# Optimization experiments

Measured on AMD Instinct MI355X. Metric: run time of the kernel, lower is better.

The kernel has to match this reference:

```python
import jax, jax.numpy as jnp
import numpy as np

L, D, H, DFF, P, B = 10, 512, 8, 1536, 16, 1024
DK = D // H
SQRT_DK = float(np.sqrt(DK))

# board geometry constants (square index -> rank/file/diag)
_pos = np.arange(64)
FILES = _pos % 8
RANKS = _pos // 8
DIAGS = RANKS + FILES
ADIAGS = RANKS - FILES + 7
RIDX = np.clip(RANKS[:, None] - RANKS[None, :], -7, 7) + 7  # [64,64]
FIDX = np.clip(FILES[:, None] - FILES[None, :], -7, 7) + 7  # [64,64]


def setup_inputs() -> dict:
    key = jax.random.key(0)
    ks = iter(jax.random.split(key, 40))
    n = lambda shape, s=0.02: (jax.random.normal(next(ks), shape, jnp.float32) * s)
    inp = {
        'x': jax.random.normal(next(ks), (B, 64, P), jnp.float32),
        'emb_W': n((P, D)), 'emb_b': jnp.zeros((D,), jnp.float32),
        'cls': n((1, 1, D)), 'abs_pos': n((1, 64, D)),
        'file_tab': n((8, D)), 'rank_tab': n((8, D)),
        'diag_tab': n((15, D)), 'anti_tab': n((15, D)),
        'rel_bias': n((L, 15, 15, H)),
        'Wq': n((L, D, D)), 'bq': jnp.zeros((L, D)),
        'Wk': n((L, D, D)), 'bk': jnp.zeros((L, D)),
        'Wv': n((L, D, D)), 'bv': jnp.zeros((L, D)),
        'Wo': n((L, D, D)), 'bo': jnp.zeros((L, D)),
        'ln1_g': jnp.ones((L, D)), 'ln1_b': jnp.zeros((L, D)),
        'ln2_g': jnp.ones((L, D)), 'ln2_b': jnp.zeros((L, D)),
        'W1': n((L, D, 2 * DFF)), 'b1': jnp.zeros((L, 2 * DFF)),
        'W2': n((L, DFF, D)), 'b2': jnp.zeros((L, D)),
        'fln_g': jnp.ones((D,)), 'fln_b': jnp.zeros((D,)),
        'pol_W': n((D, 72)), 'pol_b': jnp.zeros((72,)),
        'v1_W': n((D, D // 2)), 'v1_b': jnp.zeros((D // 2,)),
        'v2_W': n((D // 2, 128)), 'v2_b': jnp.zeros((128,)),
        'v3_W': n((128, 1)), 'v3_b': jnp.zeros((1,)),
    }
    return inp


def _ln(x, g, b):
    m = x.mean(-1, keepdims=True)
    v = ((x - m) ** 2).mean(-1, keepdims=True)
    return (x - m) * jax.lax.rsqrt(v + 1e-5) * g + b


def _gelu(x):
    return jax.nn.gelu(x, approximate=False)  # torch F.gelu default (erf)


def reference(x, emb_W, emb_b, cls, abs_pos, file_tab, rank_tab, diag_tab, anti_tab,
              rel_bias, Wq, bq, Wk, bk, Wv, bv, Wo, bo, ln1_g, ln1_b, ln2_g, ln2_b,
              W1, b1, W2, b2, fln_g, fln_b, pol_W, pol_b,
              v1_W, v1_b, v2_W, v2_b, v3_W, v3_b):
    Bn = x.shape[0]
    # per-square embedding + chess positional encoding
    emb = x @ emb_W + emb_b                                   # [B,64,D]
    pe = abs_pos + file_tab[FILES] + rank_tab[RANKS] + diag_tab[DIAGS] + anti_tab[ADIAGS]
    t = emb + pe
    t = jnp.concatenate([jnp.broadcast_to(cls, (Bn, 1, D)), t], axis=1)  # [B,65,D]
    for i in range(L):
        h = _ln(t, ln1_g[i], ln1_b[i])
        q = (h @ Wq[i] + bq[i]).reshape(Bn, 65, H, DK).transpose(0, 2, 1, 3)
        k = (h @ Wk[i] + bk[i]).reshape(Bn, 65, H, DK).transpose(0, 2, 1, 3)
        v = (h @ Wv[i] + bv[i]).reshape(Bn, 65, H, DK).transpose(0, 2, 1, 3)
        scores = jnp.einsum('bhqd,bhkd->bhqk', q, k) / SQRT_DK
        bias = rel_bias[i][RIDX, FIDX]                        # [64,64,H]
        bias = jnp.pad(bias.transpose(2, 0, 1), ((0, 0), (1, 0), (1, 0)))  # zero bias for CLS
        scores = scores + bias[None]
        a = jax.nn.softmax(scores, axis=-1)
        ctx = jnp.einsum('bhqk,bhkd->bhqd', a, v).transpose(0, 2, 1, 3).reshape(Bn, 65, D)
        t = t + (ctx @ Wo[i] + bo[i])
        h = _ln(t, ln2_g[i], ln2_b[i])
        p = h @ W1[i] + b1[i]
        x1, x2 = jnp.split(p, 2, axis=-1)
        t = t + (_gelu(x1) * x2) @ W2[i] + b2[i]
    t = _ln(t, fln_g, fln_b)
    policy = (t[:, 1:] @ pol_W + pol_b).reshape(Bn, -1)       # [B,4608]
    vh = t[:, 0]                                              # CLS token
    value = jnp.tanh(_gelu(_gelu(vh @ v1_W + v1_b) @ v2_W + v2_b) @ v3_W + v3_b)  # [B,1]
    return policy, value
```

## Files before the change

### kernel.cpp

```cpp
#include <hip/hip_runtime.h>
#include <hip/hip_bf16.h>
#include <math.h>


typedef short short8 __attribute__((ext_vector_type(8)));
typedef float f32x4 __attribute__((ext_vector_type(4)));

#define NLAYER 10
#define DMODEL 512
#define NHEAD 8
#define BATCH 1024
#define SEQ 65

#define WT_QKV   0L
#define WT_WO    7864320L
#define WT_W1    10485760L
#define WT_W2    26214400L
#define WT_BQKV  34078720L
#define WT_BO    34094080L
#define WT_B1    34099200L
#define WT_B2    34129920L
#define WT_POL   34135040L
#define WT_BPOL  34200576L
#define WT_TOTAL 34200704L

__device__ __forceinline__ float bf2f(ushort u){ return __uint_as_float(((unsigned)u)<<16); }
__device__ __forceinline__ ushort f2bf(float f){
  unsigned u = __float_as_uint(f);
  unsigned r = (u + 0x7fffu + ((u>>16)&1u)) >> 16;
  return (ushort)r;
}
__device__ __forceinline__ float gelu_exact(float x){
  return 0.5f*x*(1.0f+erff(x*0.70710678118654752440f));
}
__device__ __forceinline__ void gl16(ushort* lds, const ushort* g){
  __builtin_amdgcn_global_load_lds(
      (const unsigned int __attribute__((address_space(1)))*)g,
      (unsigned int __attribute__((address_space(3)))*)lds,
      16, 0, 0);
}
__device__ __forceinline__ int xcd_swizzle(int orig, int nwg){
  int q8 = nwg>>3, r8 = nwg&7;
  int xcd = orig&7, off = orig>>3;
  int base = (xcd<r8) ? xcd*(q8+1) : r8*(q8+1) + (xcd-r8)*q8;
  return base + off;
}

__global__ void prep_qkv(const float* __restrict__ Wq, const float* __restrict__ Wk,
                         const float* __restrict__ Wv, ushort* __restrict__ wT)
{
  long idx = (long)blockIdx.x*256 + threadIdx.x;
  if(idx >= 7864320L) return;
  int l = (int)(idx/786432L);
  long r = idx - (long)l*786432L;
  int n = (int)(r>>9), k = (int)(r&511);
  float v;
  if(n<512)       v = Wq[(long)l*262144 + (long)k*512 + n];
  else if(n<1024) v = Wk[(long)l*262144 + (long)k*512 + (n-512)];
  else            v = Wv[(long)l*262144 + (long)k*512 + (n-1024)];
  wT[WT_QKV + idx] = f2bf(v);
}
__global__ void prep_wo(const float* __restrict__ Wo, ushort* __restrict__ wT)
{
  long idx = (long)blockIdx.x*256 + threadIdx.x;
  if(idx >= 2621440L) return;
  int l = (int)(idx/262144L);
  long r = idx - (long)l*262144L;
  int n = (int)(r>>9), k = (int)(r&511);
  wT[WT_WO + idx] = f2bf(Wo[(long)l*262144 + (long)k*512 + n]);
}
__global__ void prep_w1(const float* __restrict__ W1, ushort* __restrict__ wT)
{
  long idx = (long)blockIdx.x*256 + threadIdx.x;
  if(idx >= 15728640L) return;
  int l = (int)(idx/1572864L);
  long r = idx - (long)l*1572864L;
  int n = (int)(r>>9), k = (int)(r&511);
  int j = n>>1;
  int src = (n&1) ? 1536+j : j;
  wT[WT_W1 + idx] = f2bf(W1[(long)l*1572864 + (long)k*3072 + src]);
}
__global__ void prep_w2(const float* __restrict__ W2, ushort* __restrict__ wT)
{
  long idx = (long)blockIdx.x*256 + threadIdx.x;
  if(idx >= 7864320L) return;
  int l = (int)(idx/786432L);
  long r = idx - (long)l*786432L;
  int n = (int)(r/1536), k = (int)(r - (long)n*1536);
  wT[WT_W2 + idx] = f2bf(W2[(long)l*786432 + (long)k*512 + n]);
}
__global__ void prep_bias(const float* __restrict__ bq, const float* __restrict__ bk,
                          const float* __restrict__ bv, const float* __restrict__ bo,
                          const float* __restrict__ b1, const float* __restrict__ b2,
                          ushort* __restrict__ wT)
{
  int idx = blockIdx.x*256 + threadIdx.x;
  if(idx >= 56320) return;
  long o = WT_BQKV + idx;
  float v;
  if(o < WT_BO){
    int i = idx;
    int l = i/1536, n = i - l*1536;
    if(n<512) v=bq[l*512+n]; else if(n<1024) v=bk[l*512+n-512]; else v=bv[l*512+n-1024];
  } else if(o < WT_B1){
    int i = (int)(o - WT_BO);
    v = bo[i];
  } else if(o < WT_B2){
    int i = (int)(o - WT_B1);
    int l = i/3072, n = i - l*3072;
    int j=n>>1; int src=(n&1)?1536+j:j;
    v = b1[l*3072+src];
  } else {
    int i = (int)(o - WT_B2);
    v = b2[i];
  }
  wT[o] = f2bf(v);
}
__global__ void prep_pol(const float* __restrict__ pol_W, const float* __restrict__ pol_b,
                         ushort* __restrict__ wT)
{
  int idx = blockIdx.x*256 + threadIdx.x;
  if(idx >= 65536+128) return;
  if(idx < 65536){
    int n = idx>>9, k = idx&511;
    wT[WT_POL + idx] = f2bf(n<72 ? pol_W[k*72+n] : 0.0f);
  } else {
    int n = idx - 65536;
    wT[WT_BPOL + n] = f2bf(n<72 ? pol_b[n] : 0.0f);
  }
}

__global__ __launch_bounds__(256) void embed_kernel(
    const float* __restrict__ x, const float* __restrict__ emb_W,
    const float* __restrict__ emb_b, const float* __restrict__ cls,
    const float* __restrict__ abs_pos, const float* __restrict__ file_tab,
    const float* __restrict__ rank_tab, const float* __restrict__ diag_tab,
    const float* __restrict__ anti_tab, float* __restrict__ t, long xoff)
{
  long tok = (long)blockIdx.x*4 + (threadIdx.x>>6);
  int lane = threadIdx.x&63;
  long b = tok/SEQ;
  int s = (int)(tok - b*SEQ);
  float* out = t + tok*DMODEL;
  if(s==0){
    #pragma unroll
    for(int j=0;j<8;j++){ int d=lane*8+j; out[d]=cls[d]; }
    return;
  }
  int p = s-1;
  int f = p&7, r = p>>3;
  int dg = r+f, ad = r-f+7;
  float xv[16];
  #pragma unroll
  for(int k=0;k<16;k++) xv[k]=x[xoff + (b*64+p)*16+k];
  #pragma unroll
  for(int j=0;j<8;j++){
    int d = lane*8+j;
    float acc = emb_b[d] + abs_pos[p*512+d] + file_tab[f*512+d]
              + rank_tab[r*512+d] + diag_tab[dg*512+d] + anti_tab[ad*512+d];
    #pragma unroll
    for(int k=0;k<16;k++) acc += xv[k]*emb_W[k*512+d];
    out[d]=acc;
  }
}

__global__ __launch_bounds__(256) void ln_kernel(const float* __restrict__ t, ushort* __restrict__ h,
                                                 const float* __restrict__ g, const float* __restrict__ b,
                                                 long goff)
{
  long tok = (long)blockIdx.x*4 + (threadIdx.x>>6);
  int lane = threadIdx.x&63;
  const float* row = t + tok*DMODEL;
  float4 v0 = *reinterpret_cast<const float4*>(row + lane*8);
  float4 v1 = *reinterpret_cast<const float4*>(row + lane*8 + 4);
  float x[8] = {v0.x,v0.y,v0.z,v0.w,v1.x,v1.y,v1.z,v1.w};
  float s=0.f, ss=0.f;
  #pragma unroll
  for(int j=0;j<8;j++){ s+=x[j]; ss+=x[j]*x[j]; }
  #pragma unroll
  for(int off=32;off>=1;off>>=1){ s+=__shfl_down(s,off); ss+=__shfl_down(ss,off); }
  s=__shfl(s,0); ss=__shfl(ss,0);
  float mean = s*(1.0f/512.0f);
  float var  = ss*(1.0f/512.0f) - mean*mean;
  float rs = rsqrtf(fmaxf(var,0.0f) + 1e-5f);
  #pragma unroll
  for(int j=0;j<8;j++){
    int d=lane*8+j;
    h[tok*DMODEL+d] = f2bf((x[j]-mean)*rs*g[goff+d] + b[goff+d]);
  }
}

template<int EPI>
__global__ __launch_bounds__(256,2) void gemm_bt(
    const ushort* __restrict__ A, long lda,
    const ushort* __restrict__ BT,
    const ushort* __restrict__ bias,
    ushort* __restrict__ Cb, float* __restrict__ Cf,
    long ldc, int K)
{
  __shared__ __align__(16) ushort As[128*64];
  __shared__ __align__(16) ushort Bs[128*64];
  const int tid = threadIdx.x;
  const int w = tid>>6, lane = tid&63, q = lane>>4, lr = lane&15;
  const int wm = (w>>1)*64, wn = (w&1)*64;

  const int nwg  = (int)(gridDim.x*gridDim.y);
  const int orig = (int)(blockIdx.y*gridDim.x + blockIdx.x);
  const int wgid = xcd_swizzle(orig, nwg);
  const int bxx  = wgid % (int)gridDim.x, byy = wgid / (int)gridDim.x;
  const long mBase = (long)byy*128, nBase = (long)bxx*128;

  f32x4 acc[4][4];
  #pragma unroll
  for(int i=0;i<4;i++)
    #pragma unroll
    for(int j=0;j<4;j++) acc[i][j]=(f32x4)(0.0f);

  const int ar = tid>>3, ac = (tid&7)*8;
  const ushort* gA = A  + (mBase+ar)*lda     + ac;
  const ushort* gB = BT + (nBase+ar)*(long)K + ac;
  ushort* lA = As + tid*8;
  ushort* lB = Bs + tid*8;

  for(int k0=0;k0<K;k0+=64){
    __syncthreads();
    #pragma unroll
    for(int i=0;i<4;i++){
      gl16(lA + i*2048, gA + (long)(i*32)*lda + k0);
      gl16(lB + i*2048, gB + (long)(i*32)*K   + k0);
    }
    __syncthreads();
    #pragma unroll
    for(int ks=0;ks<2;ks++){
      short8 af[4], bfr[4];
      #pragma unroll
      for(int mt=0;mt<4;mt++) af[mt]=*reinterpret_cast<const short8*>(As + (wm+mt*16+lr)*64 + ks*32 + q*8);
      #pragma unroll
      for(int nt=0;nt<4;nt++) bfr[nt]=*reinterpret_cast<const short8*>(Bs + (wn+nt*16+lr)*64 + ks*32 + q*8);
      #pragma unroll
      for(int mt=0;mt<4;mt++)
        #pragma unroll
        for(int nt=0;nt<4;nt++)
          acc[mt][nt]=__builtin_amdgcn_mfma_f32_16x16x32_bf16(af[mt],bfr[nt],acc[mt][nt],0,0,0);
    }
  }

  #pragma unroll
  for(int nt=0;nt<4;nt++){
    long n = nBase+wn+nt*16+lr;
    float bv = bf2f(bias[n]);
    #pragma unroll
    for(int mt=0;mt<4;mt++){
      #pragma unroll
      for(int r=0;r<4;r++){
        long m = mBase+wm+mt*16+q*4+r;
        float v = acc[mt][nt][r]+bv;
        if constexpr (EPI==0){
          Cb[m*ldc+n]=f2bf(v);
        } else if constexpr (EPI==1){
          Cf[m*ldc+n]+=v;
        } else if constexpr (EPI==2){
          float partner = __shfl_xor(v,1);
          if(!(lane&1)) Cb[m*ldc + (n>>1)] = f2bf(gelu_exact(v)*partner);
        } else {
          long bl = m/65;
          int p = (int)(m - bl*65) - 1;
          if(p>=0 && n<72) Cf[bl*4608 + (long)p*72 + n] = v;
        }
      }
    }
  }
}

__global__ __launch_bounds__(256) void attn_kernel(const ushort* __restrict__ qkv,
                                                   const float* __restrict__ rel_bias,
                                                   ushort* __restrict__ ctx, int layer)
{
  int bh = blockIdx.x;
  long b = bh>>3;
  int h = bh&7;
  __shared__ __align__(16) ushort QKP[11520];
  __shared__ __align__(16) ushort Vt[64*104];
  __shared__ __align__(16) float  S [65*65];
  __shared__ float relb[225];
  ushort* Qb = QKP;
  ushort* Kb = QKP + 5760;
  ushort* Pb = QKP;
  const long tokBase = b*SEQ;
  const int tid = threadIdx.x;
  const int w = tid>>6, lane = tid&63, q = lane>>4, lr = lane&15;

  for(int idx=tid; idx<SEQ*8; idx+=256){
    int s = idx>>3, c8 = (idx&7)<<3;
    long base = (tokBase+s)*1536 + h*64 + c8;
    *reinterpret_cast<short8*>(&Qb[s*72 + c8]) = *reinterpret_cast<const short8*>(&qkv[base]);
    *reinterpret_cast<short8*>(&Kb[s*72 + c8]) = *reinterpret_cast<const short8*>(&qkv[base+512]);
    short8 v = *reinterpret_cast<const short8*>(&qkv[base+1024]);
    #pragma unroll
    for(int j=0;j<8;j++) Vt[(c8+j)*104 + s] = (ushort)v[j];
  }
  for(int idx=tid; idx<64*32; idx+=256){
    int d = idx>>5, s = 65+(idx&31);
    Vt[d*104 + s] = 0;
  }
  if(tid<225) relb[tid] = rel_bias[((long)layer*225 + tid)*8 + h];
  __syncthreads();

  for(int tt=w; tt<25; tt+=4){
    int mt = tt/5, nt = tt - mt*5;
    f32x4 acc = (f32x4)(0.0f);
    #pragma unroll
    for(int ks=0;ks<2;ks++){
      short8 af = *reinterpret_cast<const short8*>(&Qb[(mt*16+lr)*72 + ks*32 + q*8]);
      short8 bf = *reinterpret_cast<const short8*>(&Kb[(nt*16+lr)*72 + ks*32 + q*8]);
      acc = __builtin_amdgcn_mfma_f32_16x16x32_bf16(af, bf, acc, 0,0,0);
    }
    int col = nt*16 + lr;
    if(col < SEQ){
      #pragma unroll
      for(int r=0;r<4;r++){
        int row = mt*16 + q*4 + r;
        if(row < SEQ) S[row*65 + col] = acc[r]*0.125f;
      }
    }
  }
  __syncthreads();

  {
    int grp = tid>>2, sub = tid&3;
    for(int qi=grp; qi<SEQ; qi+=64){
      float* srow = S + qi*65;
      int pq = qi-1;
      float mx = -1e30f;
      for(int k=sub;k<SEQ;k+=4){
        float s = srow[k];
        if(qi>0 && k>0){
          int pk = k-1;
          int ridx = (pq>>3)-(pk>>3)+7, fidx = (pq&7)-(pk&7)+7;
          s += relb[ridx*15+fidx];
        }
        srow[k] = s;
        mx = fmaxf(mx, s);
      }
      mx = fmaxf(mx, __shfl_xor(mx,1));
      mx = fmaxf(mx, __shfl_xor(mx,2));
      float sum = 0.f;
      for(int k=sub;k<SEQ;k+=4){ float e = __expf(srow[k]-mx); srow[k]=e; sum+=e; }
      sum += __shfl_xor(sum,1);
      sum += __shfl_xor(sum,2);
      float inv = 1.0f/sum;
      ushort* prow = Pb + qi*104;
      for(int k=sub;k<SEQ;k+=4) prow[k] = f2bf(srow[k]*inv);
      for(int k=SEQ+sub;k<96;k+=4) prow[k] = 0;
    }
  }
  __syncthreads();

  for(int tt=w; tt<20; tt+=4){
    int mt = tt>>2, nt = tt&3;
    f32x4 acc = (f32x4)(0.0f);
    #pragma unroll
    for(int ks=0;ks<3;ks++){
      short8 af = *reinterpret_cast<const short8*>(&Pb[(mt*16+lr)*104 + ks*32 + q*8]);
      short8 bf = *reinterpret_cast<const short8*>(&Vt[(nt*16+lr)*104 + ks*32 + q*8]);
      acc = __builtin_amdgcn_mfma_f32_16x16x32_bf16(af, bf, acc, 0,0,0);
    }
    int col = nt*16 + lr;
    #pragma unroll
    for(int r=0;r<4;r++){
      int row = mt*16 + q*4 + r;
      if(row < SEQ)
        ctx[(tokBase+row)*512 + h*64 + col] = f2bf(acc[r]);
    }
  }
}

__global__ __launch_bounds__(256) void value_kernel(const ushort* __restrict__ h,
                                                    const float* __restrict__ v1_W, const float* __restrict__ v1_b,
                                                    const float* __restrict__ v2_W, const float* __restrict__ v2_b,
                                                    const float* __restrict__ v3_W, const float* __restrict__ v3_b,
                                                    float* __restrict__ out, long b0)
{
  long bl = blockIdx.x;
  int tid = threadIdx.x;
  __shared__ float vh[512], a1[256], a2[128];
  const ushort* hrow = h + bl*SEQ*DMODEL;
  for(int d=tid; d<512; d+=256) vh[d]=bf2f(hrow[d]);
  __syncthreads();
  {
    float acc = v1_b[tid];
    for(int k=0;k<512;k++) acc += vh[k]*v1_W[k*256+tid];
    a1[tid]=gelu_exact(acc);
  }
  __syncthreads();
  if(tid<128){
    float acc = v2_b[tid];
    for(int k=0;k<256;k++) acc += a1[k]*v2_W[k*128+tid];
    a2[tid]=gelu_exact(acc);
  }
  __syncthreads();
  if(tid==0){
    float acc = v3_b[0];
    for(int k=0;k<128;k++) acc += a2[k]*v3_W[k];
    out[(long)BATCH*4608 + b0 + bl] = tanhf(acc);
  }
}

extern "C" void kernel_launch(void* const* d_in, const int* in_sizes, int n_in,
                              void* d_out, int out_size, void* d_ws, size_t ws_size,
                              hipStream_t stream)
{
  const float* x        = (const float*)d_in[0];
  const float* emb_W    = (const float*)d_in[1];
  const float* emb_b    = (const float*)d_in[2];
  const float* cls      = (const float*)d_in[3];
  const float* abs_pos  = (const float*)d_in[4];
  const float* file_tab = (const float*)d_in[5];
  const float* rank_tab = (const float*)d_in[6];
  const float* diag_tab = (const float*)d_in[7];
  const float* anti_tab = (const float*)d_in[8];
  const float* rel_bias = (const float*)d_in[9];
  const float* Wq  = (const float*)d_in[10];
  const float* bq  = (const float*)d_in[11];
  const float* Wk  = (const float*)d_in[12];
  const float* bk  = (const float*)d_in[13];
  const float* Wv  = (const float*)d_in[14];
  const float* bv  = (const float*)d_in[15];
  const float* Wo  = (const float*)d_in[16];
  const float* bo  = (const float*)d_in[17];
  const float* ln1_g = (const float*)d_in[18];
  const float* ln1_b = (const float*)d_in[19];
  const float* ln2_g = (const float*)d_in[20];
  const float* ln2_b = (const float*)d_in[21];
  const float* W1  = (const float*)d_in[22];
  const float* b1  = (const float*)d_in[23];
  const float* W2  = (const float*)d_in[24];
  const float* b2  = (const float*)d_in[25];
  const float* fln_g = (const float*)d_in[26];
  const float* fln_b = (const float*)d_in[27];
  const float* pol_W = (const float*)d_in[28];
  const float* pol_b = (const float*)d_in[29];
  const float* v1_W  = (const float*)d_in[30];
  const float* v1_b  = (const float*)d_in[31];
  const float* v2_W  = (const float*)d_in[32];
  const float* v2_b  = (const float*)d_in[33];
  const float* v3_W  = (const float*)d_in[34];
  const float* v3_b  = (const float*)d_in[35];
  float* out = (float*)d_out;

  int nchunk = 4;
  if(ws_size >= (size_t)477345792) nchunk = 1;
  else if(ws_size >= (size_t)272873472) nchunk = 2;
  const int bch = BATCH / nchunk;
  const long mch = (long)bch * SEQ;

  char* ws = (char*)d_ws;
  float*  t    = (float*)ws;  ws += (size_t)mch*DMODEL*4;
  ushort* h    = (ushort*)ws; ws += (size_t)mch*DMODEL*2;
  ushort* buf1 = (ushort*)ws; ws += (size_t)mch*1536*2;
  ushort* wT   = (ushort*)ws; ws += (size_t)WT_TOTAL*2;
  (void)ws_size; (void)in_sizes; (void)n_in; (void)out_size;

  prep_qkv<<<(7864320+255)/256,256,0,stream>>>(Wq,Wk,Wv,wT);
  prep_wo <<<(2621440+255)/256,256,0,stream>>>(Wo,wT);
  prep_w1 <<<(15728640+255)/256,256,0,stream>>>(W1,wT);
  prep_w2 <<<(7864320+255)/256,256,0,stream>>>(W2,wT);
  prep_bias<<<(56320+255)/256,256,0,stream>>>(bq,bk,bv,bo,b1,b2,wT);
  prep_pol <<<(65664+255)/256,256,0,stream>>>(pol_W,pol_b,wT);

  const int gy = (int)(mch/128);
  const int lng = (int)(mch/4);
  for(int c=0;c<nchunk;c++){
    long b0 = (long)c*bch;
    embed_kernel<<<lng,256,0,stream>>>(x, emb_W, emb_b, cls, abs_pos,
                                      file_tab, rank_tab, diag_tab, anti_tab, t, b0*64*16);
    for(int l=0;l<NLAYER;l++){
      ln_kernel<<<lng,256,0,stream>>>(t, h, ln1_g, ln1_b, l*512);
      gemm_bt<0><<<dim3(12,gy),256,0,stream>>>(h, 512, wT+WT_QKV+(long)l*786432,
                                                wT+WT_BQKV+l*1536, buf1, nullptr, 1536, 512);
      attn_kernel<<<bch*NHEAD,256,0,stream>>>(buf1, rel_bias, h, l);
      gemm_bt<1><<<dim3(4,gy),256,0,stream>>>(h, 512, wT+WT_WO+(long)l*262144,
                                               wT+WT_BO+l*512, nullptr, t, 512, 512);
      ln_kernel<<<lng,256,0,stream>>>(t, h, ln2_g, ln2_b, l*512);
      gemm_bt<2><<<dim3(24,gy),256,0,stream>>>(h, 512, wT+WT_W1+(long)l*1572864,
                                                wT+WT_B1+l*3072, buf1, nullptr, 1536, 512);
      gemm_bt<1><<<dim3(4,gy),256,0,stream>>>(buf1, 1536, wT+WT_W2+(long)l*786432,
                                               wT+WT_B2+l*512, nullptr, t, 512, 1536);
    }
    ln_kernel<<<lng,256,0,stream>>>(t, h, fln_g, fln_b, 0);
    gemm_bt<3><<<dim3(1,gy),256,0,stream>>>(h, 512, wT+WT_POL,
                                            wT+WT_BPOL, nullptr, out + b0*4608, 0, 512);
    value_kernel<<<bch,256,0,stream>>>(h, v1_W, v1_b, v2_W, v2_b, v3_W, v3_b, out, b0);
  }
}
```

Measured before the change: 12.44 ms.

## Double-buffer LDS tiles in bf16 GEMM to overlap loads with MFMA

Shared-memory A and B tiles in the GEMM kernel become two ping-pong buffers. The next K-tile's global-to-LDS loads are issued before computing on the current one, and one of the two barriers per iteration is removed. The aim is to hide global load latency behind MFMA work. The cost is doubled LDS use per block (64KB), which may limit how many blocks fit per CU.

```diff
diff --git a/kernel.cpp b/kernel.cpp
--- a/kernel.cpp
+++ b/kernel.cpp
@@ -198,8 +198,8 @@
     ushort* __restrict__ Cb, float* __restrict__ Cf,
     long ldc, int K)
 {
-  __shared__ __align__(16) ushort As[128*64];
-  __shared__ __align__(16) ushort Bs[128*64];
+  __shared__ __align__(16) ushort As[2][128*64];
+  __shared__ __align__(16) ushort Bs[2][128*64];
   const int tid = threadIdx.x;
   const int w = tid>>6, lane = tid&63, q = lane>>4, lr = lane&15;
   const int wm = (w>>1)*64, wn = (w&1)*64;
@@ -219,24 +219,29 @@
   const int ar = tid>>3, ac = (tid&7)*8;
   const ushort* gA = A  + (mBase+ar)*lda     + ac;
   const ushort* gB = BT + (nBase+ar)*(long)K + ac;
-  ushort* lA = As + tid*8;
-  ushort* lB = Bs + tid*8;
-
-  for(int k0=0;k0<K;k0+=64){
+
+  #define STAGE(bf,k0) do{                                          \
+    _Pragma("unroll")                                               \
+    for(int i_=0;i_<4;i_++){                                        \
+      gl16(&As[bf][tid*8 + i_*2048], gA + (long)(i_*32)*lda + (k0));\
+      gl16(&Bs[bf][tid*8 + i_*2048], gB + (long)(i_*32)*K   + (k0));\
+    } }while(0)
+
+  const int NT = K>>6;
+  STAGE(0, 0);
+
+  for(int t=0;t<NT;t++){
     __syncthreads();
-    #pragma unroll
-    for(int i=0;i<4;i++){
-      gl16(lA + i*2048, gA + (long)(i*32)*lda + k0);
-      gl16(lB + i*2048, gB + (long)(i*32)*K   + k0);
-    }
-    __syncthreads();
+    if(t+1<NT) STAGE((t+1)&1, (t+1)<<6);
+    const ushort* Asb = As[t&1];
+    const ushort* Bsb = Bs[t&1];
     #pragma unroll
     for(int ks=0;ks<2;ks++){
       short8 af[4], bfr[4];
       #pragma unroll
-      for(int mt=0;mt<4;mt++) af[mt]=*reinterpret_cast<const short8*>(As + (wm+mt*16+lr)*64 + ks*32 + q*8);
+      for(int mt=0;mt<4;mt++) af[mt]=*reinterpret_cast<const short8*>(Asb + (wm+mt*16+lr)*64 + ks*32 + q*8);
       #pragma unroll
-      for(int nt=0;nt<4;nt++) bfr[nt]=*reinterpret_cast<const short8*>(Bs + (wn+nt*16+lr)*64 + ks*32 + q*8);
+      for(int nt=0;nt<4;nt++) bfr[nt]=*reinterpret_cast<const short8*>(Bsb + (wn+nt*16+lr)*64 + ks*32 + q*8);
       #pragma unroll
       for(int mt=0;mt<4;mt++)
         #pragma unroll
@@ -244,6 +249,7 @@
           acc[mt][nt]=__builtin_amdgcn_mfma_f32_16x16x32_bf16(af[mt],bfr[nt],acc[mt][nt],0,0,0);
     }
   }
+  #undef STAGE
 
   #pragma unroll
   for(int nt=0;nt<4;nt++){
```

New measurement: 15.89 ms. +27.8%, slower.
